# Kernel tuning notes

Measured on AMD Instinct MI355X. Metric: run time of the kernel, lower is better.

## Reference

```python
import jax, jax.numpy as jnp
import numpy as np

V, D, NL = 32000, 768, 4
DI, N, DC, DTR = 2 * D, 16, 4, 48  # d_inner, d_state, d_conv, dt_rank
B, L = 2, 1024


def _rmsnorm(x, w, eps=1e-5):
    var = jnp.mean(x * x, axis=-1, keepdims=True)
    return x * jax.lax.rsqrt(var + eps) * w


def _causal_depthwise_conv(x, w, b):
    # x: (B, L, DI), w: (DI, DC), b: (DI,)
    xc = x.transpose(0, 2, 1)  # (B, DI, L)
    out = jax.lax.conv_general_dilated(
        xc, w[:, None, :], window_strides=(1,), padding=[(DC - 1, 0)],
        dimension_numbers=("NCH", "OIH", "NCH"), feature_group_count=DI)
    return (out + b[None, :, None]).transpose(0, 2, 1)


def _selective_scan(u, delta, A, Bm, Cm, Dv):
    # u,delta: (B,L,DI); A: (DI,N); Bm,Cm: (B,L,N); Dv: (DI,)
    dA = jnp.exp(delta[..., None] * A)                       # (B,L,DI,N)
    dBu = delta[..., None] * Bm[:, :, None, :] * u[..., None]  # (B,L,DI,N)

    def step(h, inp):
        dA_t, dBu_t, C_t = inp
        h = dA_t * h + dBu_t                                  # (B,DI,N)
        y = jnp.einsum("bdn,bn->bd", h, C_t)
        return h, y

    h0 = jnp.zeros((u.shape[0], DI, N), u.dtype)
    _, ys = jax.lax.scan(step, h0, (dA.transpose(1, 0, 2, 3),
                                    dBu.transpose(1, 0, 2, 3),
                                    Cm.transpose(1, 0, 2)))
    return ys.transpose(1, 0, 2) + u * Dv


def _mamba_block(x, norm_w, in_w, conv_w, conv_b, xproj_w, dt_w, dt_b,
                 A_log, Dv, out_w):
    xn = _rmsnorm(x, norm_w)
    xz = jnp.einsum("bld,ed->ble", xn, in_w)                 # (B,L,2*DI)
    xb, z = jnp.split(xz, 2, axis=-1)
    xb = jax.nn.silu(_causal_depthwise_conv(xb, conv_w, conv_b))
    x_dbl = jnp.einsum("bld,ed->ble", xb, xproj_w)           # (B,L,DTR+2N)
    dt, Bm, Cm = jnp.split(x_dbl, [DTR, DTR + N], axis=-1)
    delta = jax.nn.softplus(jnp.einsum("blr,dr->bld", dt, dt_w) + dt_b)
    y = _selective_scan(xb, delta, -jnp.exp(A_log), Bm, Cm, Dv)
    y = y * jax.nn.silu(z)
    return x + jnp.einsum("ble,de->bld", y, out_w)


def setup_inputs() -> dict:
    key = jax.random.key(0)
    ks = jax.random.split(key, 16)
    s = lambda k, shape, sc=0.02: jax.random.normal(k, shape, jnp.float32) * sc
    dt_init = jnp.log(jnp.expm1(
        jnp.exp(jax.random.uniform(ks[12], (NL, DI), jnp.float32,
                                   np.log(1e-3), np.log(1e-1)))))
    return {
        "tokens": jax.random.randint(ks[0], (B, L), 0, V),
        "embedding": s(ks[1], (V, D)),
        "W_out_w": s(ks[2], (V, D)),
        "W_out_b": jnp.zeros((V,), jnp.float32),
        "norm_w": jnp.ones((NL, D), jnp.float32),
        "in_proj_w": s(ks[3], (NL, 2 * DI, D)),
        "conv_w": s(ks[4], (NL, DI, DC), 0.1),
        "conv_b": jnp.zeros((NL, DI), jnp.float32),
        "x_proj_w": s(ks[5], (NL, DTR + 2 * N, DI)),
        "dt_proj_w": s(ks[6], (NL, DI, DTR), 0.1),
        "dt_proj_b": dt_init,
        "A_log": jnp.log(jnp.broadcast_to(
            jnp.arange(1, N + 1, dtype=jnp.float32), (NL, DI, N))),
        "D": jnp.ones((NL, DI), jnp.float32),
        "out_proj_w": s(ks[7], (NL, D, DI)),
    }


def reference(tokens, embedding, W_out_w, W_out_b, norm_w, in_proj_w,
              conv_w, conv_b, x_proj_w, dt_proj_w, dt_proj_b, A_log, D,
              out_proj_w):
    x = embedding[tokens]                                    # (B,L,D)
    for i in range(NL):
        x = _mamba_block(x, norm_w[i], in_proj_w[i], conv_w[i], conv_b[i],
                         x_proj_w[i], dt_proj_w[i], dt_proj_b[i],
                         A_log[i], D[i], out_proj_w[i])
    return jnp.einsum("bld,vd->blv", x, W_out_w) + W_out_b
```

## Files before the change

kernel.cpp:

```cpp
#include <hip/hip_runtime.h>
#include <hip/hip_bf16.h>
#include <math.h>

#define BB   2
#define LL   1024
#define DD   768
#define DIN  1536
#define NS   16
#define DCV  4
#define DTRK 48
#define NLAY 4
#define VV   32000
#define ROWS (BB*LL)

#define NCH  32
#define CLEN (LL/NCH)

typedef __attribute__((ext_vector_type(8))) short short8;
typedef __attribute__((ext_vector_type(4))) float f32x4;


__global__ __launch_bounds__(256) void embed_kernel(
    const int* __restrict__ tok, const float* __restrict__ emb,
    float* __restrict__ x) {
  int idx = blockIdx.x * 256 + threadIdx.x;
  int row = idx / DD, c = idx - row * DD;
  x[idx] = emb[(size_t)tok[row] * DD + c];
}

__global__ __launch_bounds__(256) void cvt_bf16_kernel(
    const float* __restrict__ in, __hip_bfloat16* __restrict__ out, int n4) {
  int i = blockIdx.x * 256 + threadIdx.x;
  if (i >= n4) return;
  float4 v = ((const float4*)in)[i];
  __hip_bfloat16 t0 = __float2bfloat16(v.x);
  __hip_bfloat16 t1 = __float2bfloat16(v.y);
  __hip_bfloat16 t2 = __float2bfloat16(v.z);
  __hip_bfloat16 t3 = __float2bfloat16(v.w);
  ushort4 pack = make_ushort4(*(unsigned short*)&t0, *(unsigned short*)&t1,
                              *(unsigned short*)&t2, *(unsigned short*)&t3);
  ((ushort4*)out)[i] = pack;
}

__global__ __launch_bounds__(256) void rmsnorm_kernel(
    const float* __restrict__ x, const float* __restrict__ w,
    __hip_bfloat16* __restrict__ xn) {
  int row = blockIdx.x;
  int t = threadIdx.x;
  const float* xr = x + (size_t)row * DD;
  float v0 = xr[t], v1 = xr[t + 256], v2 = xr[t + 512];
  float ss = v0 * v0 + v1 * v1 + v2 * v2;
#pragma unroll
  for (int off = 32; off > 0; off >>= 1) ss += __shfl_down(ss, off);
  __shared__ float sred[4];
  if ((t & 63) == 0) sred[t >> 6] = ss;
  __syncthreads();
  float tot = sred[0] + sred[1] + sred[2] + sred[3];
  float scale = rsqrtf(tot * (1.0f / DD) + 1e-5f);
  __hip_bfloat16* xo = xn + (size_t)row * DD;
  xo[t]       = __float2bfloat16(v0 * scale * w[t]);
  xo[t + 256] = __float2bfloat16(v1 * scale * w[t + 256]);
  xo[t + 512] = __float2bfloat16(v2 * scale * w[t + 512]);
}

__global__ __launch_bounds__(256) void conv_silu_kernel(
    const float* __restrict__ xz, const float* __restrict__ cw,
    const float* __restrict__ cb, float* __restrict__ xb) {
  int idx = blockIdx.x * 256 + threadIdx.x;
  int row = idx / DIN;
  int d = idx - row * DIN;
  int l = row & (LL - 1);
  const float* col = xz + (size_t)row * (2 * DIN) + d;
  float w0 = cw[d * 4 + 0], w1 = cw[d * 4 + 1], w2 = cw[d * 4 + 2],
        w3 = cw[d * 4 + 3];
  float acc = cb[d] + w3 * col[0];
  if (l >= 1) acc += w2 * col[-(2 * DIN)];
  if (l >= 2) acc += w1 * col[-2 * (2 * DIN)];
  if (l >= 3) acc += w0 * col[-3 * (2 * DIN)];
  float sig = 1.0f / (1.0f + __expf(-acc));
  xb[idx] = acc * sig;
}

__device__ __forceinline__ float softplus_f(float t) {
  return t > 20.0f ? t : log1pf(__expf(t));
}

template <int EPI>
__global__ __launch_bounds__(256) void sgemm_nt(
    const float* __restrict__ A, int lda,
    const float* __restrict__ W, int ldw,
    float* __restrict__ C, int ldc,
    int N, int K, const float* __restrict__ bias) {
  __shared__ float As[16][68];
  __shared__ float Ws[16][68];
  const int tid = threadIdx.x;
  const int tx = tid & 15, ty = tid >> 4;
  const int bm = blockIdx.x, bn = blockIdx.y;
  const int lrow = tid >> 2;
  const int lk4 = (tid & 3) << 2;
  const float* Aptr = A + (size_t)(bm * 64 + lrow) * lda + lk4;
  const int wrow = bn * 64 + lrow;
  const float* Wptr = W + (size_t)wrow * ldw + lk4;
  const bool wvalid = wrow < N;
  float c[4][4] = {};
  for (int k0 = 0; k0 < K; k0 += 16) {
    float4 a4 = *(const float4*)(Aptr + k0);
    float4 w4 = wvalid ? *(const float4*)(Wptr + k0) : make_float4(0, 0, 0, 0);
    __syncthreads();
    As[lk4 + 0][lrow] = a4.x; As[lk4 + 1][lrow] = a4.y;
    As[lk4 + 2][lrow] = a4.z; As[lk4 + 3][lrow] = a4.w;
    Ws[lk4 + 0][lrow] = w4.x; Ws[lk4 + 1][lrow] = w4.y;
    Ws[lk4 + 2][lrow] = w4.z; Ws[lk4 + 3][lrow] = w4.w;
    __syncthreads();
#pragma unroll
    for (int k = 0; k < 16; k++) {
      float4 a = *(const float4*)&As[k][ty << 2];
      float4 w = *(const float4*)&Ws[k][tx << 2];
      c[0][0] += a.x * w.x; c[0][1] += a.x * w.y; c[0][2] += a.x * w.z; c[0][3] += a.x * w.w;
      c[1][0] += a.y * w.x; c[1][1] += a.y * w.y; c[1][2] += a.y * w.z; c[1][3] += a.y * w.w;
      c[2][0] += a.z * w.x; c[2][1] += a.z * w.y; c[2][2] += a.z * w.z; c[2][3] += a.z * w.w;
      c[3][0] += a.w * w.x; c[3][1] += a.w * w.y; c[3][2] += a.w * w.z; c[3][3] += a.w * w.w;
    }
  }
  const int m0 = bm * 64 + (ty << 2);
  const int n0 = bn * 64 + (tx << 2);
#pragma unroll
  for (int i = 0; i < 4; i++) {
    float* crow = C + (size_t)(m0 + i) * ldc;
#pragma unroll
    for (int j = 0; j < 4; j++) {
      int n = n0 + j;
      if (n < N) {
        float v = c[i][j];
        if constexpr (EPI == 1) v = softplus_f(v + bias[n]);
        crow[n] = v;
      }
    }
  }
}


__device__ __forceinline__ void gload16(const void* g, void* l) {
  __builtin_amdgcn_global_load_lds(
      (const __attribute__((address_space(1))) void*)g,
      (__attribute__((address_space(3))) void*)l, 16, 0, 0);
}

template <int EPI>
__global__ __launch_bounds__(256) void bgemm_nt(
    const __hip_bfloat16* __restrict__ A, int lda,
    const __hip_bfloat16* __restrict__ W, int ldw,
    float* __restrict__ C, int ldc,
    int K, const float* __restrict__ bias) {
  __shared__ short As[128 * 32];
  __shared__ short Ws[128 * 32];
  const int tid = threadIdx.x;
  const int wave = tid >> 6, lane = tid & 63;
  const int wm = wave >> 1, wn = wave & 1;
  const int tileM = blockIdx.x * 128, tileN = blockIdx.y * 128;

  const short* Ag = (const short*)A;
  const short* Wg = (const short*)W;
  const int cid0 = tid, cid1 = tid + 256;
  const size_t aOff0 = (size_t)(tileM + (cid0 >> 2)) * lda + (cid0 & 3) * 8;
  const size_t aOff1 = (size_t)(tileM + (cid1 >> 2)) * lda + (cid1 & 3) * 8;
  const size_t wOff0 = (size_t)(tileN + (cid0 >> 2)) * ldw + (cid0 & 3) * 8;
  const size_t wOff1 = (size_t)(tileN + (cid1 >> 2)) * ldw + (cid1 & 3) * 8;
  short* AsD0 = As + wave * 512;
  short* AsD1 = As + 2048 + wave * 512;
  short* WsD0 = Ws + wave * 512;
  short* WsD1 = Ws + 2048 + wave * 512;

  const int fr = lane & 15, fq = lane >> 4;
  f32x4 acc[4][4] = {};

  for (int k0 = 0; k0 < K; k0 += 32) {
    gload16(Ag + aOff0 + k0, AsD0);
    gload16(Ag + aOff1 + k0, AsD1);
    gload16(Wg + wOff0 + k0, WsD0);
    gload16(Wg + wOff1 + k0, WsD1);
    __syncthreads();
    short8 afr[4], bfr[4];
#pragma unroll
    for (int t = 0; t < 4; t++) {
      afr[t] = *(const short8*)(As + (wm * 64 + t * 16 + fr) * 32 + fq * 8);
      bfr[t] = *(const short8*)(Ws + (wn * 64 + t * 16 + fr) * 32 + fq * 8);
    }
#pragma unroll
    for (int mt = 0; mt < 4; mt++)
#pragma unroll
      for (int nt = 0; nt < 4; nt++)
        acc[mt][nt] = __builtin_amdgcn_mfma_f32_16x16x32_bf16(
            afr[mt], bfr[nt], acc[mt][nt], 0, 0, 0);
    __syncthreads();
  }

#pragma unroll
  for (int mt = 0; mt < 4; mt++) {
#pragma unroll
    for (int r = 0; r < 4; r++) {
      int row = tileM + wm * 64 + mt * 16 + fq * 4 + r;
      float* crow = C + (size_t)row * ldc;
#pragma unroll
      for (int nt = 0; nt < 4; nt++) {
        int col = tileN + wn * 64 + nt * 16 + fr;
        float v = acc[mt][nt][r];
        if constexpr (EPI == 2) v += crow[col];
        else if constexpr (EPI == 3) v += bias[col];
        crow[col] = v;
      }
    }
  }
}


__global__ __launch_bounds__(256) void scan_pass1(
    const float* __restrict__ u,
    const float* __restrict__ dlt,
    const float* __restrict__ xdbl,
    const float* __restrict__ A_log,
    float* __restrict__ qbuf,
    float* __restrict__ sdel) {
  const int d = blockIdx.x * 256 + threadIdx.x;
  const int c = blockIdx.y;
  const int b = blockIdx.z;
  float Ac2[NS];
  {
    const float* ar = A_log + (size_t)d * NS;
#pragma unroll
    for (int j = 0; j < NS; j++) Ac2[j] = -__expf(ar[j]) * 1.44269504f;
  }
  const int l0 = c * CLEN;
  const float* ur = u   + ((size_t)b * LL + l0) * DIN + d;
  const float* dr = dlt + ((size_t)b * LL + l0) * DIN + d;
  const float* br = xdbl + ((size_t)b * LL + l0) * 80 + DTRK;
  float h[NS];
#pragma unroll
  for (int j = 0; j < NS; j++) h[j] = 0.0f;
  float sd = 0.0f;
  for (int t = 0; t < CLEN; t++) {
    float dl = dr[(size_t)t * DIN];
    float ul = ur[(size_t)t * DIN];
    float Bv[NS];
    *(float4*)&Bv[0]  = *(const float4*)(br + (size_t)t * 80);
    *(float4*)&Bv[4]  = *(const float4*)(br + (size_t)t * 80 + 4);
    *(float4*)&Bv[8]  = *(const float4*)(br + (size_t)t * 80 + 8);
    *(float4*)&Bv[12] = *(const float4*)(br + (size_t)t * 80 + 12);
    sd += dl;
    float du = dl * ul;
#pragma unroll
    for (int j = 0; j < NS; j++)
      h[j] = exp2f(dl * Ac2[j]) * h[j] + du * Bv[j];
  }
  float* qo = qbuf + (((size_t)b * NCH + c) * DIN + d) * NS;
#pragma unroll
  for (int j = 0; j < NS; j += 4)
    *(float4*)(qo + j) = make_float4(h[j], h[j + 1], h[j + 2], h[j + 3]);
  sdel[((size_t)b * NCH + c) * DIN + d] = sd;
}

__global__ __launch_bounds__(256) void scan_pass2(
    const float* __restrict__ qbuf, const float* __restrict__ sdel,
    const float* __restrict__ A_log, float* __restrict__ hstart) {
  const int e = blockIdx.x * 256 + threadIdx.x;
  const int n = e & (NS - 1);
  const int d = e >> 4;
  const int b = blockIdx.y;
  float Ac2 = -__expf(A_log[(size_t)d * NS + n]) * 1.44269504f;
  float h = 0.0f;
  for (int c = 0; c < NCH; c++) {
    hstart[(((size_t)b * NCH + c) * DIN + d) * NS + n] = h;
    if (c + 1 < NCH) {
      float sd = sdel[((size_t)b * NCH + c) * DIN + d];
      float q  = qbuf[(((size_t)b * NCH + c) * DIN + d) * NS + n];
      h = exp2f(Ac2 * sd) * h + q;
    }
  }
}

__global__ __launch_bounds__(256) void scan_pass3(
    const float* __restrict__ u,
    const float* __restrict__ dlt,
    const float* __restrict__ xdbl,
    const float* __restrict__ xz,
    const float* __restrict__ A_log,
    const float* __restrict__ Dv,
    const float* __restrict__ hstart,
    __hip_bfloat16* __restrict__ y) {
  const int d = blockIdx.x * 256 + threadIdx.x;
  const int c = blockIdx.y;
  const int b = blockIdx.z;
  float Ac2[NS];
  {
    const float* ar = A_log + (size_t)d * NS;
#pragma unroll
    for (int j = 0; j < NS; j++) Ac2[j] = -__expf(ar[j]) * 1.44269504f;
  }
  const float Dd = Dv[d];
  float h[NS];
  {
    const float* hs = hstart + (((size_t)b * NCH + c) * DIN + d) * NS;
#pragma unroll
    for (int j = 0; j < NS; j += 4) {
      float4 hv = *(const float4*)(hs + j);
      h[j] = hv.x; h[j + 1] = hv.y; h[j + 2] = hv.z; h[j + 3] = hv.w;
    }
  }
  const int l0 = c * CLEN;
  const float* ur = u   + ((size_t)b * LL + l0) * DIN + d;
  const float* dr = dlt + ((size_t)b * LL + l0) * DIN + d;
  const float* br = xdbl + ((size_t)b * LL + l0) * 80 + DTRK;
  const float* cr = br + NS;
  const float* zr = xz + ((size_t)b * LL + l0) * (2 * DIN) + DIN + d;
  __hip_bfloat16* yr = y + ((size_t)b * LL + l0) * DIN + d;
  for (int t = 0; t < CLEN; t++) {
    float dl = dr[(size_t)t * DIN];
    float ul = ur[(size_t)t * DIN];
    float zl = zr[(size_t)t * (2 * DIN)];
    float Bv[NS], Cv[NS];
    *(float4*)&Bv[0]  = *(const float4*)(br + (size_t)t * 80);
    *(float4*)&Bv[4]  = *(const float4*)(br + (size_t)t * 80 + 4);
    *(float4*)&Bv[8]  = *(const float4*)(br + (size_t)t * 80 + 8);
    *(float4*)&Bv[12] = *(const float4*)(br + (size_t)t * 80 + 12);
    *(float4*)&Cv[0]  = *(const float4*)(cr + (size_t)t * 80);
    *(float4*)&Cv[4]  = *(const float4*)(cr + (size_t)t * 80 + 4);
    *(float4*)&Cv[8]  = *(const float4*)(cr + (size_t)t * 80 + 8);
    *(float4*)&Cv[12] = *(const float4*)(cr + (size_t)t * 80 + 12);
    float du = dl * ul;
    float acc = 0.0f;
#pragma unroll
    for (int j = 0; j < NS; j++) {
      h[j] = exp2f(dl * Ac2[j]) * h[j] + du * Bv[j];
      acc += h[j] * Cv[j];
    }
    acc += ul * Dd;
    float sig = 1.0f / (1.0f + __expf(-zl));
    yr[(size_t)t * DIN] = __float2bfloat16(acc * (zl * sig));
  }
}


extern "C" void kernel_launch(void* const* d_in, const int* in_sizes, int n_in,
                              void* d_out, int out_size, void* d_ws,
                              size_t ws_size, hipStream_t stream) {
  const int*   tokens    = (const int*)d_in[0];
  const float* embedding = (const float*)d_in[1];
  const float* W_out_w   = (const float*)d_in[2];
  const float* W_out_b   = (const float*)d_in[3];
  const float* norm_w    = (const float*)d_in[4];
  const float* in_proj_w = (const float*)d_in[5];
  const float* conv_w    = (const float*)d_in[6];
  const float* conv_b    = (const float*)d_in[7];
  const float* x_proj_w  = (const float*)d_in[8];
  const float* dt_proj_w = (const float*)d_in[9];
  const float* dt_proj_b = (const float*)d_in[10];
  const float* A_log     = (const float*)d_in[11];
  const float* Dvec      = (const float*)d_in[12];
  const float* out_proj_w= (const float*)d_in[13];
  float* out = (float*)d_out;

  float* ws = (float*)d_ws;
  float* x    = ws;
  float* xz   = x + (size_t)ROWS * DD;
  float* xb   = xz + (size_t)ROWS * 2 * DIN;
  float* xdbl = xb + (size_t)ROWS * DIN;
  float* dlt  = xdbl + (size_t)ROWS * 80;
  __hip_bfloat16* bfbase = (__hip_bfloat16*)(dlt + (size_t)ROWS * DIN);
  __hip_bfloat16* xnb  = bfbase;
  __hip_bfloat16* ybb  = xnb + (size_t)ROWS * DD;
  __hip_bfloat16* xbf  = ybb + (size_t)ROWS * DIN;
  __hip_bfloat16* wInB = xbf + (size_t)ROWS * DD;
  __hip_bfloat16* wOpB = wInB + (size_t)NLAY * 2 * DIN * DD;
  __hip_bfloat16* wLgB = wOpB + (size_t)NLAY * DD * DIN;
  float* qbuf   = (float*)(wLgB + (size_t)VV * DD);
  float* sdel   = qbuf + (size_t)BB * NCH * DIN * NS;
  float* hstart = sdel + (size_t)BB * NCH * DIN;

  {
    int n4 = NLAY * 2 * DIN * DD / 4;
    cvt_bf16_kernel<<<(n4 + 255) / 256, 256, 0, stream>>>(in_proj_w, wInB, n4);
    n4 = NLAY * DD * DIN / 4;
    cvt_bf16_kernel<<<(n4 + 255) / 256, 256, 0, stream>>>(out_proj_w, wOpB, n4);
    n4 = VV * DD / 4;
    cvt_bf16_kernel<<<(n4 + 255) / 256, 256, 0, stream>>>(W_out_w, wLgB, n4);
  }

  embed_kernel<<<ROWS * DD / 256, 256, 0, stream>>>(tokens, embedding, x);

  for (int i = 0; i < NLAY; i++) {
    rmsnorm_kernel<<<ROWS, 256, 0, stream>>>(x, norm_w + (size_t)i * DD, xnb);
    bgemm_nt<0><<<dim3(16, 24), 256, 0, stream>>>(
        xnb, DD, wInB + (size_t)i * 2 * DIN * DD, DD, xz, 2 * DIN, DD,
        nullptr);
    conv_silu_kernel<<<ROWS * DIN / 256, 256, 0, stream>>>(
        xz, conv_w + (size_t)i * DIN * DCV, conv_b + (size_t)i * DIN, xb);
    sgemm_nt<0><<<dim3(32, 2), 256, 0, stream>>>(
        xb, DIN, x_proj_w + (size_t)i * (DTRK + 2 * NS) * DIN, DIN, xdbl,
        DTRK + 2 * NS, DTRK + 2 * NS, DIN, nullptr);
    sgemm_nt<1><<<dim3(32, 24), 256, 0, stream>>>(
        xdbl, DTRK + 2 * NS, dt_proj_w + (size_t)i * DIN * DTRK, DTRK, dlt,
        DIN, DIN, DTRK, dt_proj_b + (size_t)i * DIN);
    const float* Ai = A_log + (size_t)i * DIN * NS;
    scan_pass1<<<dim3(DIN / 256, NCH - 1, BB), 256, 0, stream>>>(
        xb, dlt, xdbl, Ai, qbuf, sdel);
    scan_pass2<<<dim3(DIN * NS / 256, BB), 256, 0, stream>>>(
        qbuf, sdel, Ai, hstart);
    scan_pass3<<<dim3(DIN / 256, NCH, BB), 256, 0, stream>>>(
        xb, dlt, xdbl, xz, Ai, Dvec + (size_t)i * DIN, hstart, ybb);
    bgemm_nt<2><<<dim3(16, 6), 256, 0, stream>>>(
        ybb, DIN, wOpB + (size_t)i * DD * DIN, DIN, x, DD, DIN, nullptr);
  }

  {
    int n4 = ROWS * DD / 4;
    cvt_bf16_kernel<<<(n4 + 255) / 256, 256, 0, stream>>>(x, xbf, n4);
  }
  bgemm_nt<3><<<dim3(16, 250), 256, 0, stream>>>(
      xbf, DD, wLgB, DD, out, VV, DD, W_out_b);
}
```

Measured before the change: 1.620 ms.

## Split-K x_proj GEMM, vectorize conv, fuse weight casts, swizzle bf16 GEMM tiles

Several independent changes. The small x_proj GEMM, previously only 64 workgroups, is split eight ways along K, with atomicAdd accumulation into a pre-zeroed output. The depthwise conv+SiLU now handles four channels per thread using float4 loads, and the three weight bf16 conversions become one grid-stride launch. The bf16 GEMM also remaps workgroup indices in groups of eight, which may improve cache locality. Risks include atomic contention and nondeterministic summation order, plus an extra zeroing kernel per layer.

```diff
diff --git a/kernel.cpp b/kernel.cpp
--- a/kernel.cpp
+++ b/kernel.cpp
@@ -28,10 +28,9 @@
   x[idx] = emb[(size_t)tok[row] * DD + c];
 }
 
-__global__ __launch_bounds__(256) void cvt_bf16_kernel(
-    const float* __restrict__ in, __hip_bfloat16* __restrict__ out, int n4) {
-  int i = blockIdx.x * 256 + threadIdx.x;
-  if (i >= n4) return;
+__device__ __forceinline__ void cvt4_bf16(const float* __restrict__ in,
+                                          __hip_bfloat16* __restrict__ out,
+                                          int i) {
   float4 v = ((const float4*)in)[i];
   __hip_bfloat16 t0 = __float2bfloat16(v.x);
   __hip_bfloat16 t1 = __float2bfloat16(v.y);
@@ -40,6 +39,30 @@
   ushort4 pack = make_ushort4(*(unsigned short*)&t0, *(unsigned short*)&t1,
                               *(unsigned short*)&t2, *(unsigned short*)&t3);
   ((ushort4*)out)[i] = pack;
+}
+
+__global__ __launch_bounds__(256) void cvt_bf16_kernel(
+    const float* __restrict__ in, __hip_bfloat16* __restrict__ out, int n4) {
+  int i = blockIdx.x * 256 + threadIdx.x;
+  if (i >= n4) return;
+  cvt4_bf16(in, out, i);
+}
+
+__global__ __launch_bounds__(256) void cvt3_bf16_kernel(
+    const float* __restrict__ i0, __hip_bfloat16* __restrict__ o0, int n0,
+    const float* __restrict__ i1, __hip_bfloat16* __restrict__ o1, int n1,
+    const float* __restrict__ i2, __hip_bfloat16* __restrict__ o2, int n2) {
+  int start = blockIdx.x * 256 + threadIdx.x;
+  int stride = gridDim.x * 256;
+  for (int j = start; j < n0; j += stride) cvt4_bf16(i0, o0, j);
+  for (int j = start; j < n1; j += stride) cvt4_bf16(i1, o1, j);
+  for (int j = start; j < n2; j += stride) cvt4_bf16(i2, o2, j);
+}
+
+__global__ __launch_bounds__(256) void zero_kernel(float* __restrict__ p,
+                                                   int n) {
+  int i = blockIdx.x * 256 + threadIdx.x;
+  if (i < n) p[i] = 0.0f;
 }
 
 __global__ __launch_bounds__(256) void rmsnorm_kernel(
@@ -67,18 +90,31 @@
     const float* __restrict__ xz, const float* __restrict__ cw,
     const float* __restrict__ cb, float* __restrict__ xb) {
   int idx = blockIdx.x * 256 + threadIdx.x;
-  int row = idx / DIN;
-  int d = idx - row * DIN;
+  int row = idx / (DIN / 4);
+  int d4 = idx - row * (DIN / 4);
+  int d = d4 << 2;
   int l = row & (LL - 1);
   const float* col = xz + (size_t)row * (2 * DIN) + d;
-  float w0 = cw[d * 4 + 0], w1 = cw[d * 4 + 1], w2 = cw[d * 4 + 2],
-        w3 = cw[d * 4 + 3];
-  float acc = cb[d] + w3 * col[0];
-  if (l >= 1) acc += w2 * col[-(2 * DIN)];
-  if (l >= 2) acc += w1 * col[-2 * (2 * DIN)];
-  if (l >= 3) acc += w0 * col[-3 * (2 * DIN)];
-  float sig = 1.0f / (1.0f + __expf(-acc));
-  xb[idx] = acc * sig;
+  float4 x0 = *(const float4*)col;
+  float4 x1 = make_float4(0, 0, 0, 0), x2 = x1, x3 = x1;
+  if (l >= 1) x1 = *(const float4*)(col - 2 * DIN);
+  if (l >= 2) x2 = *(const float4*)(col - 4 * DIN);
+  if (l >= 3) x3 = *(const float4*)(col - 6 * DIN);
+  float4 bb = *(const float4*)(cb + d);
+  float4 wa = *(const float4*)(cw + (size_t)(d + 0) * 4);
+  float4 wb = *(const float4*)(cw + (size_t)(d + 1) * 4);
+  float4 wc = *(const float4*)(cw + (size_t)(d + 2) * 4);
+  float4 wd = *(const float4*)(cw + (size_t)(d + 3) * 4);
+  float4 r;
+  r.x = bb.x + wa.w * x0.x + wa.z * x1.x + wa.y * x2.x + wa.x * x3.x;
+  r.y = bb.y + wb.w * x0.y + wb.z * x1.y + wb.y * x2.y + wb.x * x3.y;
+  r.z = bb.z + wc.w * x0.z + wc.z * x1.z + wc.y * x2.z + wc.x * x3.z;
+  r.w = bb.w + wd.w * x0.w + wd.z * x1.w + wd.y * x2.w + wd.x * x3.w;
+  r.x = r.x / (1.0f + __expf(-r.x));
+  r.y = r.y / (1.0f + __expf(-r.y));
+  r.z = r.z / (1.0f + __expf(-r.z));
+  r.w = r.w / (1.0f + __expf(-r.w));
+  *(float4*)(xb + (size_t)row * DIN + d) = r;
 }
 
 __device__ __forceinline__ float softplus_f(float t) {
@@ -96,6 +132,9 @@
   const int tid = threadIdx.x;
   const int tx = tid & 15, ty = tid >> 4;
   const int bm = blockIdx.x, bn = blockIdx.y;
+  const int kLen = K / gridDim.z;
+  const int kBegin = blockIdx.z * kLen;
+  const int kEnd = kBegin + kLen;
   const int lrow = tid >> 2;
   const int lk4 = (tid & 3) << 2;
   const float* Aptr = A + (size_t)(bm * 64 + lrow) * lda + lk4;
@@ -103,7 +142,7 @@
   const float* Wptr = W + (size_t)wrow * ldw + lk4;
   const bool wvalid = wrow < N;
   float c[4][4] = {};
-  for (int k0 = 0; k0 < K; k0 += 16) {
+  for (int k0 = kBegin; k0 < kEnd; k0 += 16) {
     float4 a4 = *(const float4*)(Aptr + k0);
     float4 w4 = wvalid ? *(const float4*)(Wptr + k0) : make_float4(0, 0, 0, 0);
     __syncthreads();
@@ -124,6 +163,7 @@
   }
   const int m0 = bm * 64 + (ty << 2);
   const int n0 = bn * 64 + (tx << 2);
+  const bool split = gridDim.z > 1;
 #pragma unroll
   for (int i = 0; i < 4; i++) {
     float* crow = C + (size_t)(m0 + i) * ldc;
@@ -133,7 +173,8 @@
       if (n < N) {
         float v = c[i][j];
         if constexpr (EPI == 1) v = softplus_f(v + bias[n]);
-        crow[n] = v;
+        if (split) atomicAdd(&crow[n], v);
+        else crow[n] = v;
       }
     }
   }
@@ -157,7 +198,15 @@
   const int tid = threadIdx.x;
   const int wave = tid >> 6, lane = tid & 63;
   const int wm = wave >> 1, wn = wave & 1;
-  const int tileM = blockIdx.x * 128, tileN = blockIdx.y * 128;
+
+  const int nbx = gridDim.x;
+  const int nwg = nbx * gridDim.y;
+  int flat = blockIdx.y * nbx + blockIdx.x;
+  if ((nwg & 7) == 0) {
+    int chunk = nwg >> 3;
+    flat = (flat & 7) * chunk + (flat >> 3);
+  }
+  const int tileM = (flat % nbx) * 128, tileN = (flat / nbx) * 128;
 
   const short* Ag = (const short*)A;
   const short* Wg = (const short*)W;
@@ -376,14 +425,10 @@
   float* sdel   = qbuf + (size_t)BB * NCH * DIN * NS;
   float* hstart = sdel + (size_t)BB * NCH * DIN;
 
-  {
-    int n4 = NLAY * 2 * DIN * DD / 4;
-    cvt_bf16_kernel<<<(n4 + 255) / 256, 256, 0, stream>>>(in_proj_w, wInB, n4);
-    n4 = NLAY * DD * DIN / 4;
-    cvt_bf16_kernel<<<(n4 + 255) / 256, 256, 0, stream>>>(out_proj_w, wOpB, n4);
-    n4 = VV * DD / 4;
-    cvt_bf16_kernel<<<(n4 + 255) / 256, 256, 0, stream>>>(W_out_w, wLgB, n4);
-  }
+  cvt3_bf16_kernel<<<2048, 256, 0, stream>>>(
+      in_proj_w, wInB, NLAY * 2 * DIN * DD / 4,
+      out_proj_w, wOpB, NLAY * DD * DIN / 4,
+      W_out_w, wLgB, VV * DD / 4);
 
   embed_kernel<<<ROWS * DD / 256, 256, 0, stream>>>(tokens, embedding, x);
 
@@ -392,9 +437,10 @@
     bgemm_nt<0><<<dim3(16, 24), 256, 0, stream>>>(
         xnb, DD, wInB + (size_t)i * 2 * DIN * DD, DD, xz, 2 * DIN, DD,
         nullptr);
-    conv_silu_kernel<<<ROWS * DIN / 256, 256, 0, stream>>>(
+    conv_silu_kernel<<<ROWS * DIN / 4 / 256, 256, 0, stream>>>(
         xz, conv_w + (size_t)i * DIN * DCV, conv_b + (size_t)i * DIN, xb);
-    sgemm_nt<0><<<dim3(32, 2), 256, 0, stream>>>(
+    zero_kernel<<<ROWS * 80 / 256, 256, 0, stream>>>(xdbl, ROWS * 80);
+    sgemm_nt<0><<<dim3(32, 2, 8), 256, 0, stream>>>(
         xb, DIN, x_proj_w + (size_t)i * (DTRK + 2 * NS) * DIN, DIN, xdbl,
         DTRK + 2 * NS, DTRK + 2 * NS, DIN, nullptr);
     sgemm_nt<1><<<dim3(32, 24), 256, 0, stream>>>(
```

Result: faster. 1.398 ms (-13.7%).
